# Kernel tuning notes

Measured on AMD Instinct MI355X. Metric: run time of the kernel, lower is better.

Reference implementation:

```python
import jax, jax.numpy as jnp
import numpy as np

B, T, E, H = 2, 2048, 768, 12
HD = E // H  # 64


def setup_inputs() -> dict:
    key = jax.random.key(0)
    ks = jax.random.split(key, 5)
    s = 0.02
    return {
        "token_embeddings": jax.random.normal(ks[0], (B, T, E), dtype=jnp.float32),
        "W_Q": jax.random.normal(ks[1], (E, E), dtype=jnp.float32) * s,
        "W_K": jax.random.normal(ks[2], (E, E), dtype=jnp.float32) * s,
        "W_V": jax.random.normal(ks[3], (E, E), dtype=jnp.float32) * s,
        "W_pool": jax.random.normal(ks[4], (E, E), dtype=jnp.float32) * s,
    }


def reference(token_embeddings, W_Q, W_K, W_V, W_pool):
    # torch Linear (bias=False): y = x @ W.T with W of shape (out, in)
    Q = token_embeddings @ W_Q.T
    K = token_embeddings @ W_K.T
    V = token_embeddings @ W_V.T
    # Faithful replication of the module's unusual head split:
    # contiguous view (B, T, E) -> (B, H, T, HD), NOT the standard split+transpose.
    Q = Q.reshape(B, H, T, HD)
    K = K.reshape(B, H, T, HD)
    V = V.reshape(B, H, T, HD)
    scores = jnp.einsum("bhqd,bhkd->bhqk", Q, K)  # [B,H,T,T]
    causal = jnp.tril(jnp.ones((T, T), dtype=bool))
    scores = jnp.where(causal, scores, -jnp.inf)
    attn = jax.nn.softmax(scores / jnp.float32(np.sqrt(HD)), axis=-1)
    out = jnp.einsum("bhqk,bhkd->bhqd", attn, V)  # [B,H,T,HD]
    # Faithful: transpose(1,2) then contiguous view back to (B, T, E)
    out = jnp.transpose(out, (0, 2, 1, 3)).reshape(B, T, E)
    return out @ W_pool.T
```

## Files before the change

kernel.cpp:

```cpp
#include <hip/hip_runtime.h>

typedef unsigned short u16;
typedef unsigned int u32;
typedef __attribute__((ext_vector_type(8))) short bf16x8;
typedef __attribute__((ext_vector_type(4))) float f32x4;
typedef __attribute__((ext_vector_type(4))) unsigned short u16x4;
typedef __attribute__((ext_vector_type(2))) unsigned int u32x2;

#define GM 4096
#define GN 768
#define GK 768
#define NITEMS 768
#define QSCALE 0.18033688011112042f

static __device__ __forceinline__ u16 f2bf(float f) {
  union { float f; unsigned u; } v; v.f = f;
  unsigned u = v.u;
  return (u16)((u + 0x7FFFu + ((u >> 16) & 1u)) >> 16);
}

static __device__ __forceinline__ float exp2_hw(float x) {
  float r;
  asm("v_exp_f32 %0, %1" : "=v"(r) : "v"(x));
  return r;
}

static __device__ __forceinline__ u32 pack_rn(float lo, float hi) {
  u32 a = __float_as_uint(lo) + 0x8000u;
  u32 b = __float_as_uint(hi) + 0x8000u;
  return (a >> 16) | (b & 0xFFFF0000u);
}

static __device__ __forceinline__ void gld16(const void* g, void* l) {
  __builtin_amdgcn_global_load_lds((__attribute__((address_space(1))) void*)(g),
                                   (__attribute__((address_space(3))) void*)(l),
                                   16, 0, 0);
}

__global__ void cvt_bf16(const float* __restrict__ in, u16* __restrict__ out, int n4) {
  int i = blockIdx.x * blockDim.x + threadIdx.x;
  if (i < n4) {
    float4 v = ((const float4*)in)[i];
    u16x4 o;
    o[0] = f2bf(v.x); o[1] = f2bf(v.y); o[2] = f2bf(v.z); o[3] = f2bf(v.w);
    ((u16x4*)out)[i] = o;
  }
}

__global__ void cvt_w4(const float* __restrict__ w0, const float* __restrict__ w1,
                       const float* __restrict__ w2, const float* __restrict__ w3,
                       u16* __restrict__ o0, u16* __restrict__ o1,
                       u16* __restrict__ o2, u16* __restrict__ o3, int n4) {
  const float* in = blockIdx.y == 0 ? w0 : (blockIdx.y == 1 ? w1 : (blockIdx.y == 2 ? w2 : w3));
  u16* out = blockIdx.y == 0 ? o0 : (blockIdx.y == 1 ? o1 : (blockIdx.y == 2 ? o2 : o3));
  int i = blockIdx.x * blockDim.x + threadIdx.x;
  if (i < n4) {
    float4 v = ((const float4*)in)[i];
    u16x4 o;
    o[0] = f2bf(v.x); o[1] = f2bf(v.y); o[2] = f2bf(v.z); o[3] = f2bf(v.w);
    ((u16x4*)out)[i] = o;
  }
}

template<int F32OUT>
static __device__ __forceinline__ void gemm_core(const u16* __restrict__ A,
                                                 const u16* __restrict__ B,
                                                 void* __restrict__ O,
                                                 u16* lA, u16* lB, float scale)
{
  const int tid = threadIdx.x;
  const int wave = tid >> 6, lane = tid & 63;
  const int g = lane >> 4, c = lane & 15;
  const int wr = (wave >> 1) * 64, wc = (wave & 1) * 64;
  const int tm = blockIdx.x * 128, tn = blockIdx.y * 128;

  f32x4 acc[4][4] = {};

  const int srow = lane >> 2;
  const int scolb = (lane & 3) * 16;
  const char* gA = (const char*)(A + (size_t)tm * GK);
  const char* gB = (const char*)(B + (size_t)tn * GK);

  for (int k0 = 0; k0 < GK; k0 += 32) {
#pragma unroll
    for (int i = 0; i < 2; ++i) {
      const int chunk = wave * 2 + i;
      const int row = chunk * 16 + srow;
      gld16(gA + (size_t)row * (GK * 2) + k0 * 2 + scolb, (char*)lA + chunk * 1024);
      gld16(gB + (size_t)row * (GK * 2) + k0 * 2 + scolb, (char*)lB + chunk * 1024);
    }
    __syncthreads();
    bf16x8 af[4], bfr[4];
#pragma unroll
    for (int m = 0; m < 4; ++m)
      af[m] = *(const bf16x8*)((const char*)lA + (wr + m * 16 + c) * 64 + g * 16);
#pragma unroll
    for (int n = 0; n < 4; ++n)
      bfr[n] = *(const bf16x8*)((const char*)lB + (wc + n * 16 + c) * 64 + g * 16);
#pragma unroll
    for (int m = 0; m < 4; ++m)
#pragma unroll
      for (int n = 0; n < 4; ++n)
        acc[m][n] = __builtin_amdgcn_mfma_f32_16x16x32_bf16(af[m], bfr[n], acc[m][n], 0, 0, 0);
    __syncthreads();
  }

#pragma unroll
  for (int m = 0; m < 4; ++m)
#pragma unroll
    for (int n = 0; n < 4; ++n) {
      const int row0 = tm + wr + m * 16 + g * 4;
      const int col = tn + wc + n * 16 + c;
#pragma unroll
      for (int r = 0; r < 4; ++r) {
        if (F32OUT)
          ((float*)O)[(size_t)(row0 + r) * GN + col] = acc[m][n][r];
        else
          ((u16*)O)[(size_t)(row0 + r) * GN + col] = f2bf(acc[m][n][r] * scale);
      }
    }
}

__global__ __launch_bounds__(256) void gemm_qkv(const u16* __restrict__ A,
    const u16* __restrict__ B0, const u16* __restrict__ B1, const u16* __restrict__ B2,
    u16* __restrict__ O0, u16* __restrict__ O1, u16* __restrict__ O2)
{
  __shared__ u16 lA[4096], lB[4096];
  const u16* B = blockIdx.z == 0 ? B0 : (blockIdx.z == 1 ? B1 : B2);
  u16* O = blockIdx.z == 0 ? O0 : (blockIdx.z == 1 ? O1 : O2);
  const float scale = blockIdx.z == 0 ? QSCALE : 1.0f;
  gemm_core<0>(A, B, O, lA, lB, scale);
}

__global__ __launch_bounds__(256) void gemm_pool(const u16* __restrict__ A,
    const u16* __restrict__ B, float* __restrict__ O)
{
  __shared__ u16 lA[4096], lB[4096];
  gemm_core<1>(A, B, O, lA, lB, 1.0f);
}

__global__ __launch_bounds__(256) void vtrans(const u16* __restrict__ V, u16* __restrict__ VT) {
  const int tblk = blockIdx.x;
  const int bh = blockIdx.y;
  __shared__ u16 tile[64][72];
  const u16* Vh = V + (size_t)bh * 131072;
  u16* Vt = VT + (size_t)bh * 131072;
  const int tid = threadIdx.x;
  const int t0 = tblk * 64;
#pragma unroll
  for (int i = 0; i < 4; ++i) {
    int idx = i * 256 + tid;
    int row = idx >> 4;
    int c4 = idx & 15;
    u16x4 v = *(const u16x4*)(Vh + (size_t)(t0 + row) * 64 + c4 * 4);
    tile[row][c4 * 4 + 0] = v[0]; tile[row][c4 * 4 + 1] = v[1];
    tile[row][c4 * 4 + 2] = v[2]; tile[row][c4 * 4 + 3] = v[3];
  }
  __syncthreads();
#pragma unroll
  for (int i = 0; i < 4; ++i) {
    int idx = i * 256 + tid;
    int d = idx >> 4;
    int t4 = idx & 15;
    u16x4 o;
    o[0] = tile[t4 * 4 + 0][d]; o[1] = tile[t4 * 4 + 1][d];
    o[2] = tile[t4 * 4 + 2][d]; o[3] = tile[t4 * 4 + 3][d];
    *(u16x4*)(Vt + (size_t)d * 2048 + t0 + t4 * 4) = o;
  }
}

static __device__ __forceinline__ void stage_tile(const char* gbase, int rowstride,
                                                  char* lbuf, int wave, int lane) {
#pragma unroll
  for (int i = 0; i < 2; ++i) {
    const int chunk = i * 256 + wave * 64 + lane;
    const int row = chunk >> 3;
    const int colb = (chunk & 7) << 4;
    const char* src = gbase + (size_t)row * rowstride + (colb ^ ((row & 7) << 4));
    char* dst = lbuf + i * 4096 + wave * 1024;
    gld16(src, dst);
  }
}

__global__ __launch_bounds__(256, 4) void attn(const u16* __restrict__ Q,
                                               const u16* __restrict__ Km,
                                               const u16* __restrict__ VT,
                                               u16* __restrict__ X2,
                                               u32* __restrict__ qcount)
{
  const int tid = threadIdx.x, wave = tid >> 6, lane = tid & 63;
  const int g = lane >> 4, c = lane & 15;
  const int swr = (c & 7) << 4;
  const int swz = ((c & 7) ^ (c >> 3)) << 4;

  __shared__ char Kl[2][8192];
  __shared__ char Vl[2][8192];
  __shared__ u16 Plds[4][1024];
  __shared__ int s_item;
  u16* pl = Plds[wave];

  for (;;) {
    if (tid == 0) s_item = (int)atomicAdd(qcount, 1u);
    __syncthreads();
    const int w = s_item;
    if (w >= NITEMS) return;
    const int qblk = 31 - (w / 24);
    const int bh = w % 24;
    const int b = bh / 12, h = bh % 12;

    const char* Khb = (const char*)(Km + (size_t)bh * 131072);
    const char* Vhb = (const char*)(VT + (size_t)bh * 131072);
    const u16* Qh = Q + (size_t)bh * 131072;

    const int q0 = qblk * 64 + wave * 16;
    const int nkt = qblk + 1;

    stage_tile(Khb, 128, Kl[0], wave, lane);
    stage_tile(Vhb, 4096, Vl[0], wave, lane);

    bf16x8 qf[2];
#pragma unroll
    for (int kk = 0; kk < 2; ++kk)
      qf[kk] = *(const bf16x8*)(Qh + (size_t)(q0 + c) * 64 + kk * 32 + g * 8);

    f32x4 oacc[4] = {};
    float lsum = 0.f;

    __syncthreads();

    for (int kt = 0; kt < nkt; ++kt) {
      const int cur = kt & 1;
      if (kt + 1 < nkt) {
        stage_tile(Khb + (size_t)(kt + 1) * 8192, 128, Kl[cur ^ 1], wave, lane);
        stage_tile(Vhb + (size_t)(kt + 1) * 128, 4096, Vl[cur ^ 1], wave, lane);
      }
      f32x4 s[4] = {};
      __builtin_amdgcn_s_setprio(1);
#pragma unroll
      for (int kk = 0; kk < 2; ++kk)
#pragma unroll
        for (int n = 0; n < 4; ++n) {
          bf16x8 kf = *(const bf16x8*)(Kl[cur] + (size_t)(n * 16 + c) * 128 + ((kk * 64 + g * 16) ^ swr));
          s[n] = __builtin_amdgcn_mfma_f32_16x16x32_bf16(kf, qf[kk], s[n], 0, 0, 0);
        }
      __builtin_amdgcn_s_setprio(0);
      bf16x8 vf[2][4];
#pragma unroll
      for (int kk = 0; kk < 2; ++kk)
#pragma unroll
        for (int n = 0; n < 4; ++n)
          vf[kk][n] = *(const bf16x8*)(Vl[cur] + (size_t)(n * 16 + c) * 128 + ((kk * 64 + g * 16) ^ swr));
      if (kt == nkt - 1) {
        const int qrow = q0 + c;
#pragma unroll
        for (int n = 0; n < 4; ++n) {
          const int k0i = kt * 64 + n * 16 + g * 4;
          float p0 = (k0i + 0 > qrow) ? 0.f : exp2_hw(s[n][0]);
          float p1 = (k0i + 1 > qrow) ? 0.f : exp2_hw(s[n][1]);
          float p2 = (k0i + 2 > qrow) ? 0.f : exp2_hw(s[n][2]);
          float p3 = (k0i + 3 > qrow) ? 0.f : exp2_hw(s[n][3]);
          lsum += (p0 + p1) + (p2 + p3);
          u32x2 pw; pw[0] = pack_rn(p0, p1); pw[1] = pack_rn(p2, p3);
          *(u32x2*)((char*)pl + c * 128 + ((n * 32 + g * 8) ^ swz)) = pw;
        }
      } else {
#pragma unroll
        for (int n = 0; n < 4; ++n) {
          float p0 = exp2_hw(s[n][0]);
          float p1 = exp2_hw(s[n][1]);
          float p2 = exp2_hw(s[n][2]);
          float p3 = exp2_hw(s[n][3]);
          lsum += (p0 + p1) + (p2 + p3);
          u32x2 pw; pw[0] = pack_rn(p0, p1); pw[1] = pack_rn(p2, p3);
          *(u32x2*)((char*)pl + c * 128 + ((n * 32 + g * 8) ^ swz)) = pw;
        }
      }
      __builtin_amdgcn_s_setprio(1);
#pragma unroll
      for (int kk = 0; kk < 2; ++kk) {
        bf16x8 pa = *(const bf16x8*)((const char*)pl + c * 128 + ((kk * 64 + g * 16) ^ swz));
#pragma unroll
        for (int n = 0; n < 4; ++n)
          oacc[n] = __builtin_amdgcn_mfma_f32_16x16x32_bf16(pa, vf[kk][n], oacc[n], 0, 0, 0);
      }
      __builtin_amdgcn_s_setprio(0);
      __syncthreads();
    }

    float tot = lsum;
    tot += __shfl_xor(tot, 16);
    tot += __shfl_xor(tot, 32);
    float linv[4];
#pragma unroll
    for (int r = 0; r < 4; ++r)
      linv[r] = __frcp_rn(__shfl(tot, g * 4 + r));
#pragma unroll
    for (int n = 0; n < 4; ++n)
#pragma unroll
      for (int r = 0; r < 4; ++r) {
        const float o = oacc[n][r] * linv[r];
        const int t = q0 + g * 4 + r;
        X2[((size_t)b * 2048 + t) * 768 + h * 64 + n * 16 + c] = f2bf(o);
      }
  }
}

extern "C" void kernel_launch(void* const* d_in, const int* in_sizes, int n_in,
                              void* d_out, int out_size, void* d_ws, size_t ws_size,
                              hipStream_t stream) {
  const float* x  = (const float*)d_in[0];
  const float* wq = (const float*)d_in[1];
  const float* wk = (const float*)d_in[2];
  const float* wv = (const float*)d_in[3];
  const float* wp = (const float*)d_in[4];

  const size_t SZ_X = (size_t)GM * GN * 2;
  const size_t SZ_W = (size_t)GK * GN * 2;
  char* ws = (char*)d_ws;
  u16* xbf  = (u16*)(ws);
  u16* wqb  = (u16*)(ws + SZ_X);
  u16* wkb  = (u16*)(ws + SZ_X + SZ_W);
  u16* wvb  = (u16*)(ws + SZ_X + 2 * SZ_W);
  u16* wpb  = (u16*)(ws + SZ_X + 3 * SZ_W);
  u16* Qb   = (u16*)(ws + SZ_X + 4 * SZ_W);
  u16* Kb   = (u16*)(ws + 2 * SZ_X + 4 * SZ_W);
  u16* Vb   = (u16*)(ws + 3 * SZ_X + 4 * SZ_W);
  u16* VT   = (u16*)(ws + 4 * SZ_X + 4 * SZ_W);
  u16* X2   = (u16*)(ws + 5 * SZ_X + 4 * SZ_W);
  u32* qcount = (u32*)(ws + 6 * SZ_X + 4 * SZ_W);
  if (ws_size < 6 * SZ_X + 4 * SZ_W + 256) return;

  cvt_bf16<<<dim3(3072), dim3(256), 0, stream>>>(x, xbf, GM * GN / 4);
  cvt_w4<<<dim3(576, 4), dim3(256), 0, stream>>>(wq, wk, wv, wp, wqb, wkb, wvb, wpb, GK * GN / 4);
  hipMemsetAsync(qcount, 0, sizeof(u32), stream);

  gemm_qkv<<<dim3(32, 6, 3), dim3(256), 0, stream>>>(xbf, wqb, wkb, wvb, Qb, Kb, Vb);
  vtrans<<<dim3(32, 24), dim3(256), 0, stream>>>(Vb, VT);
  attn<<<dim3(768), dim3(256), 0, stream>>>(Qb, Kb, VT, X2, qcount);
  gemm_pool<<<dim3(32, 6), dim3(256), 0, stream>>>(X2, wpb, (float*)d_out);
}
```

Baseline: 105.2 us.

## Load V fragments directly from global memory and use static attention grid

The persistent atomic work-queue scheduler is replaced with a static 2D grid indexed by query block and head, which drops the memset and the per-item atomic. The V tile is no longer staged through LDS. Each wave now reads its V fragments straight from global memory at the top of every key-tile iteration. Launch bounds rise to 6 blocks per CU, using the LDS freed by V. The changes trade the longest-first dynamic ordering and shared V reuse for lower LDS use, higher occupancy and redundant per-wave global V reads.

```diff
diff --git a/kernel.cpp b/kernel.cpp
--- a/kernel.cpp
+++ b/kernel.cpp
@@ -10,7 +10,6 @@
 #define GM 4096
 #define GN 768
 #define GK 768
-#define NITEMS 768
 #define QSCALE 0.18033688011112042f
 
 static __device__ __forceinline__ u16 f2bf(float f) {
@@ -169,140 +168,127 @@
   }
 }
 
-static __device__ __forceinline__ void stage_tile(const char* gbase, int rowstride,
-                                                  char* lbuf, int wave, int lane) {
+static __device__ __forceinline__ void stage_K(const char* gbase,
+                                               char* lbuf, int wave, int lane) {
 #pragma unroll
   for (int i = 0; i < 2; ++i) {
     const int chunk = i * 256 + wave * 64 + lane;
     const int row = chunk >> 3;
     const int colb = (chunk & 7) << 4;
-    const char* src = gbase + (size_t)row * rowstride + (colb ^ ((row & 7) << 4));
+    const char* src = gbase + (size_t)row * 128 + (colb ^ ((row & 7) << 4));
     char* dst = lbuf + i * 4096 + wave * 1024;
     gld16(src, dst);
   }
 }
 
-__global__ __launch_bounds__(256, 4) void attn(const u16* __restrict__ Q,
+__global__ __launch_bounds__(256, 6) void attn(const u16* __restrict__ Q,
                                                const u16* __restrict__ Km,
                                                const u16* __restrict__ VT,
-                                               u16* __restrict__ X2,
-                                               u32* __restrict__ qcount)
+                                               u16* __restrict__ X2)
 {
+  const int qblk = blockIdx.x;
+  const int bh = blockIdx.y;
+  const int b = bh / 12, h = bh % 12;
   const int tid = threadIdx.x, wave = tid >> 6, lane = tid & 63;
   const int g = lane >> 4, c = lane & 15;
   const int swr = (c & 7) << 4;
   const int swz = ((c & 7) ^ (c >> 3)) << 4;
 
   __shared__ char Kl[2][8192];
-  __shared__ char Vl[2][8192];
   __shared__ u16 Plds[4][1024];
-  __shared__ int s_item;
   u16* pl = Plds[wave];
 
-  for (;;) {
-    if (tid == 0) s_item = (int)atomicAdd(qcount, 1u);
+  const char* Khb = (const char*)(Km + (size_t)bh * 131072);
+  const char* Vhb = (const char*)(VT + (size_t)bh * 131072);
+  const u16* Qh = Q + (size_t)bh * 131072;
+
+  const int q0 = qblk * 64 + wave * 16;
+  const int nkt = qblk + 1;
+
+  stage_K(Khb, Kl[0], wave, lane);
+
+  bf16x8 qf[2];
+#pragma unroll
+  for (int kk = 0; kk < 2; ++kk)
+    qf[kk] = *(const bf16x8*)(Qh + (size_t)(q0 + c) * 64 + kk * 32 + g * 8);
+
+  f32x4 oacc[4] = {};
+  float lsum = 0.f;
+
+  __syncthreads();
+
+  for (int kt = 0; kt < nkt; ++kt) {
+    const int cur = kt & 1;
+    bf16x8 vf[2][4];
+#pragma unroll
+    for (int kk = 0; kk < 2; ++kk)
+#pragma unroll
+      for (int n = 0; n < 4; ++n)
+        vf[kk][n] = *(const bf16x8*)(Vhb + (size_t)(n * 16 + c) * 4096 + (kt * 64 + kk * 32 + g * 8) * 2);
+    if (kt + 1 < nkt)
+      stage_K(Khb + (size_t)(kt + 1) * 8192, Kl[cur ^ 1], wave, lane);
+    f32x4 s[4] = {};
+    __builtin_amdgcn_s_setprio(1);
+#pragma unroll
+    for (int kk = 0; kk < 2; ++kk)
+#pragma unroll
+      for (int n = 0; n < 4; ++n) {
+        bf16x8 kf = *(const bf16x8*)(Kl[cur] + (size_t)(n * 16 + c) * 128 + ((kk * 64 + g * 16) ^ swr));
+        s[n] = __builtin_amdgcn_mfma_f32_16x16x32_bf16(kf, qf[kk], s[n], 0, 0, 0);
+      }
+    __builtin_amdgcn_s_setprio(0);
+    if (kt == nkt - 1) {
+      const int qrow = q0 + c;
+#pragma unroll
+      for (int n = 0; n < 4; ++n) {
+        const int k0i = kt * 64 + n * 16 + g * 4;
+        float p0 = (k0i + 0 > qrow) ? 0.f : exp2_hw(s[n][0]);
+        float p1 = (k0i + 1 > qrow) ? 0.f : exp2_hw(s[n][1]);
+        float p2 = (k0i + 2 > qrow) ? 0.f : exp2_hw(s[n][2]);
+        float p3 = (k0i + 3 > qrow) ? 0.f : exp2_hw(s[n][3]);
+        lsum += (p0 + p1) + (p2 + p3);
+        u32x2 pw; pw[0] = pack_rn(p0, p1); pw[1] = pack_rn(p2, p3);
+        *(u32x2*)((char*)pl + c * 128 + ((n * 32 + g * 8) ^ swz)) = pw;
+      }
+    } else {
+#pragma unroll
+      for (int n = 0; n < 4; ++n) {
+        float p0 = exp2_hw(s[n][0]);
+        float p1 = exp2_hw(s[n][1]);
+        float p2 = exp2_hw(s[n][2]);
+        float p3 = exp2_hw(s[n][3]);
+        lsum += (p0 + p1) + (p2 + p3);
+        u32x2 pw; pw[0] = pack_rn(p0, p1); pw[1] = pack_rn(p2, p3);
+        *(u32x2*)((char*)pl + c * 128 + ((n * 32 + g * 8) ^ swz)) = pw;
+      }
+    }
+    __builtin_amdgcn_s_setprio(1);
+#pragma unroll
+    for (int kk = 0; kk < 2; ++kk) {
+      bf16x8 pa = *(const bf16x8*)((const char*)pl + c * 128 + ((kk * 64 + g * 16) ^ swz));
+#pragma unroll
+      for (int n = 0; n < 4; ++n)
+        oacc[n] = __builtin_amdgcn_mfma_f32_16x16x32_bf16(pa, vf[kk][n], oacc[n], 0, 0, 0);
+    }
+    __builtin_amdgcn_s_setprio(0);
     __syncthreads();
-    const int w = s_item;
-    if (w >= NITEMS) return;
-    const int qblk = 31 - (w / 24);
-    const int bh = w % 24;
-    const int b = bh / 12, h = bh % 12;
-
-    const char* Khb = (const char*)(Km + (size_t)bh * 131072);
-    const char* Vhb = (const char*)(VT + (size_t)bh * 131072);
-    const u16* Qh = Q + (size_t)bh * 131072;
-
-    const int q0 = qblk * 64 + wave * 16;
-    const int nkt = qblk + 1;
-
-    stage_tile(Khb, 128, Kl[0], wave, lane);
-    stage_tile(Vhb, 4096, Vl[0], wave, lane);
-
-    bf16x8 qf[2];
-#pragma unroll
-    for (int kk = 0; kk < 2; ++kk)
-      qf[kk] = *(const bf16x8*)(Qh + (size_t)(q0 + c) * 64 + kk * 32 + g * 8);
-
-    f32x4 oacc[4] = {};
-    float lsum = 0.f;
-
-    __syncthreads();
-
-    for (int kt = 0; kt < nkt; ++kt) {
-      const int cur = kt & 1;
-      if (kt + 1 < nkt) {
-        stage_tile(Khb + (size_t)(kt + 1) * 8192, 128, Kl[cur ^ 1], wave, lane);
-        stage_tile(Vhb + (size_t)(kt + 1) * 128, 4096, Vl[cur ^ 1], wave, lane);
-      }
-      f32x4 s[4] = {};
-      __builtin_amdgcn_s_setprio(1);
-#pragma unroll
-      for (int kk = 0; kk < 2; ++kk)
-#pragma unroll
-        for (int n = 0; n < 4; ++n) {
-          bf16x8 kf = *(const bf16x8*)(Kl[cur] + (size_t)(n * 16 + c) * 128 + ((kk * 64 + g * 16) ^ swr));
-          s[n] = __builtin_amdgcn_mfma_f32_16x16x32_bf16(kf, qf[kk], s[n], 0, 0, 0);
-        }
-      __builtin_amdgcn_s_setprio(0);
-      bf16x8 vf[2][4];
-#pragma unroll
-      for (int kk = 0; kk < 2; ++kk)
-#pragma unroll
-        for (int n = 0; n < 4; ++n)
-          vf[kk][n] = *(const bf16x8*)(Vl[cur] + (size_t)(n * 16 + c) * 128 + ((kk * 64 + g * 16) ^ swr));
-      if (kt == nkt - 1) {
-        const int qrow = q0 + c;
-#pragma unroll
-        for (int n = 0; n < 4; ++n) {
-          const int k0i = kt * 64 + n * 16 + g * 4;
-          float p0 = (k0i + 0 > qrow) ? 0.f : exp2_hw(s[n][0]);
-          float p1 = (k0i + 1 > qrow) ? 0.f : exp2_hw(s[n][1]);
-          float p2 = (k0i + 2 > qrow) ? 0.f : exp2_hw(s[n][2]);
-          float p3 = (k0i + 3 > qrow) ? 0.f : exp2_hw(s[n][3]);
-          lsum += (p0 + p1) + (p2 + p3);
-          u32x2 pw; pw[0] = pack_rn(p0, p1); pw[1] = pack_rn(p2, p3);
-          *(u32x2*)((char*)pl + c * 128 + ((n * 32 + g * 8) ^ swz)) = pw;
-        }
-      } else {
-#pragma unroll
-        for (int n = 0; n < 4; ++n) {
-          float p0 = exp2_hw(s[n][0]);
-          float p1 = exp2_hw(s[n][1]);
-          float p2 = exp2_hw(s[n][2]);
-          float p3 = exp2_hw(s[n][3]);
-          lsum += (p0 + p1) + (p2 + p3);
-          u32x2 pw; pw[0] = pack_rn(p0, p1); pw[1] = pack_rn(p2, p3);
-          *(u32x2*)((char*)pl + c * 128 + ((n * 32 + g * 8) ^ swz)) = pw;
-        }
-      }
-      __builtin_amdgcn_s_setprio(1);
-#pragma unroll
-      for (int kk = 0; kk < 2; ++kk) {
-        bf16x8 pa = *(const bf16x8*)((const char*)pl + c * 128 + ((kk * 64 + g * 16) ^ swz));
-#pragma unroll
-        for (int n = 0; n < 4; ++n)
-          oacc[n] = __builtin_amdgcn_mfma_f32_16x16x32_bf16(pa, vf[kk][n], oacc[n], 0, 0, 0);
-      }
-      __builtin_amdgcn_s_setprio(0);
-      __syncthreads();
-    }
-
-    float tot = lsum;
-    tot += __shfl_xor(tot, 16);
-    tot += __shfl_xor(tot, 32);
-    float linv[4];
-#pragma unroll
-    for (int r = 0; r < 4; ++r)
-      linv[r] = __frcp_rn(__shfl(tot, g * 4 + r));
-#pragma unroll
-    for (int n = 0; n < 4; ++n)
-#pragma unroll
-      for (int r = 0; r < 4; ++r) {
-        const float o = oacc[n][r] * linv[r];
-        const int t = q0 + g * 4 + r;
-        X2[((size_t)b * 2048 + t) * 768 + h * 64 + n * 16 + c] = f2bf(o);
-      }
-  }
+  }
+
+  float tot = lsum;
+  tot += __shfl_xor(tot, 16);
+  tot += __shfl_xor(tot, 32);
+  float linv[4];
+#pragma unroll
+  for (int r = 0; r < 4; ++r)
+    linv[r] = __frcp_rn(__shfl(tot, g * 4 + r));
+#pragma unroll
+  for (int n = 0; n < 4; ++n)
+#pragma unroll
+    for (int r = 0; r < 4; ++r) {
+      const float o = oacc[n][r] * linv[r];
+      const int t = q0 + g * 4 + r;
+      X2[((size_t)b * 2048 + t) * 768 + h * 64 + n * 16 + c] = f2bf(o);
+    }
 }
 
 extern "C" void kernel_launch(void* const* d_in, const int* in_sizes, int n_in,
@@ -327,15 +313,13 @@
   u16* Vb   = (u16*)(ws + 3 * SZ_X + 4 * SZ_W);
   u16* VT   = (u16*)(ws + 4 * SZ_X + 4 * SZ_W);
   u16* X2   = (u16*)(ws + 5 * SZ_X + 4 * SZ_W);
-  u32* qcount = (u32*)(ws + 6 * SZ_X + 4 * SZ_W);
-  if (ws_size < 6 * SZ_X + 4 * SZ_W + 256) return;
+  if (ws_size < 6 * SZ_X + 4 * SZ_W) return;
 
   cvt_bf16<<<dim3(3072), dim3(256), 0, stream>>>(x, xbf, GM * GN / 4);
   cvt_w4<<<dim3(576, 4), dim3(256), 0, stream>>>(wq, wk, wv, wp, wqb, wkb, wvb, wpb, GK * GN / 4);
-  hipMemsetAsync(qcount, 0, sizeof(u32), stream);
 
   gemm_qkv<<<dim3(32, 6, 3), dim3(256), 0, stream>>>(xbf, wqb, wkb, wvb, Qb, Kb, Vb);
   vtrans<<<dim3(32, 24), dim3(256), 0, stream>>>(Vb, VT);
-  attn<<<dim3(768), dim3(256), 0, stream>>>(Qb, Kb, VT, X2, qcount);
+  attn<<<dim3(32, 24), dim3(256), 0, stream>>>(Qb, Kb, VT, X2);
   gemm_pool<<<dim3(32, 6), dim3(256), 0, stream>>>(X2, wpb, (float*)d_out);
 }
```

New measurement: 234.9 us. +123.4%, slower.
